# Kernel tuning notes

Measured on AMD Instinct MI355X. Metric: run time of the kernel, lower is better.

## Reference

```python
import jax, jax.numpy as jnp
import numpy as np
import math

NUM_HEADS = 16
D_MODEL = 1024
B, T = 1, 4096


def setup_inputs() -> dict:
    key = jax.random.key(0)
    kx, kq, kk, kv, ko = jax.random.split(key, 5)
    s = 1.0 / math.sqrt(D_MODEL)
    return {
        "x": jax.random.normal(kx, (B, T, D_MODEL), dtype=jnp.float32),
        "Wq": jax.random.normal(kq, (D_MODEL, D_MODEL), dtype=jnp.float32) * s,
        "Wk": jax.random.normal(kk, (D_MODEL, D_MODEL), dtype=jnp.float32) * s,
        "Wv": jax.random.normal(kv, (D_MODEL, D_MODEL), dtype=jnp.float32) * s,
        "Wo": jax.random.normal(ko, (D_MODEL, D_MODEL), dtype=jnp.float32) * s,
    }


def reference(x, Wq, Wk, Wv, Wo):
    # x: (B, T, D); weights stored torch-Linear style: y = x @ W.T
    Bx, Tx, D = x.shape
    H = NUM_HEADS
    dk = D // H
    q = (x @ Wq.T).reshape(Bx, Tx, H, dk)  # (B,T,H,dk)
    k = (x @ Wk.T).reshape(Bx, Tx, H, dk)
    v = (x @ Wv.T).reshape(Bx, Tx, H, dk)
    # scores: (B,H,T,T), scaled dot-product
    scores = jnp.einsum("bthd,bshd->bhts", q, k) / math.sqrt(dk)
    causal_mask = jnp.triu(jnp.ones((Tx, Tx), dtype=bool), k=1)  # True above diag
    scores = jnp.where(causal_mask, jnp.float32(-jnp.inf), scores).astype(jnp.float32)
    attn = jax.nn.softmax(scores, axis=-1)  # fp32 softmax, as in the torch module
    out = jnp.einsum("bhts,bshd->bthd", attn, v).reshape(Bx, Tx, D)
    return out @ Wo.T
```

## Files before the change

### kernel.cpp

```cpp
#include <hip/hip_runtime.h>
#include <hip/hip_bf16.h>
#include <math.h>

typedef __attribute__((ext_vector_type(8)))  __bf16 bf16x8;
typedef __attribute__((ext_vector_type(4)))  __bf16 bf16x4;
typedef __attribute__((ext_vector_type(4)))  float  f32x4;
typedef __attribute__((ext_vector_type(16))) float  f32x16;

static constexpr int T_SEQ = 4096;
static constexpr int DM    = 1024;
static constexpr int NH    = 16;
static constexpr int SPLIT_QB   = 34;
static constexpr int SPLIT_ROWS = T_SEQ - SPLIT_QB * 64;
static constexpr float QSCALE = 0.125f * 1.44269504088896340736f;

__device__ __forceinline__ void gload16(const void* g, void* l) {
    __builtin_amdgcn_global_load_lds(
        (const __attribute__((address_space(1))) unsigned int*)g,
        (__attribute__((address_space(3))) unsigned int*)l,
        16, 0, 0);
}

__device__ __forceinline__ unsigned cvtpk_bf16(float a, float b) {
    unsigned r;
    asm("v_cvt_pk_bf16_f32 %0, %1, %2" : "=v"(r) : "v"(a), "v"(b));
    return r;
}
__device__ __forceinline__ void permswap(unsigned& x, unsigned& y) {
    asm("v_permlane32_swap_b32 %0, %1" : "+v"(x), "+v"(y));
}
__device__ __forceinline__ float xhalf_max(float v) {
    union { float f; unsigned u; } a, b;
    a.f = v; b.f = v;
    asm volatile("" : "+v"(b.u));
    permswap(a.u, b.u);
    return fmaxf(a.f, b.f);
}
__device__ __forceinline__ float xhalf_sum(float v) {
    union { float f; unsigned u; } a, b;
    a.f = v; b.f = v;
    asm volatile("" : "+v"(b.u));
    permswap(a.u, b.u);
    return a.f + b.f;
}

__global__ __launch_bounds__(256)
void cvt_bf16(const float* __restrict__ in, __bf16* __restrict__ out, int n4) {
    int i = blockIdx.x * blockDim.x + threadIdx.x;
    if (i >= n4) return;
    float4 v = ((const float4*)in)[i];
    bf16x4 o;
    o[0] = (__bf16)v.x; o[1] = (__bf16)v.y; o[2] = (__bf16)v.z; o[3] = (__bf16)v.w;
    ((bf16x4*)out)[i] = o;
}

__global__ __launch_bounds__(256)
void cvt4_bf16(const float* __restrict__ a0, const float* __restrict__ a1,
               const float* __restrict__ a2, const float* __restrict__ a3,
               __bf16* __restrict__ o0, __bf16* __restrict__ o1,
               __bf16* __restrict__ o2, __bf16* __restrict__ o3, int n4) {
    int i = blockIdx.x * blockDim.x + threadIdx.x;
    if (i >= n4) return;
    const float* in = blockIdx.y == 0 ? a0 : blockIdx.y == 1 ? a1 : blockIdx.y == 2 ? a2 : a3;
    __bf16* out     = blockIdx.y == 0 ? o0 : blockIdx.y == 1 ? o1 : blockIdx.y == 2 ? o2 : o3;
    float4 v = ((const float4*)in)[i];
    bf16x4 o;
    o[0] = (__bf16)v.x; o[1] = (__bf16)v.y; o[2] = (__bf16)v.z; o[3] = (__bf16)v.w;
    ((bf16x4*)out)[i] = o;
}

template<bool OUT_BF16>
__device__ __forceinline__ void gemm_body(const __bf16* __restrict__ A,
                                          const __bf16* __restrict__ B,
                                          void* __restrict__ Cout,
                                          int N, int K, float scale,
                                          int bx, int by) {
    __shared__ __align__(16) __bf16 Al[128 * 64];
    __shared__ __align__(16) __bf16 Bl[128 * 64];
    const int tid  = threadIdx.x;
    const int lane = tid & 63;
    const int wid  = tid >> 6;
    const int wr   = wid >> 1, wc = wid & 1;
    const int m0   = by * 128, n0 = bx * 128;
    const int r    = lane & 15, g = lane >> 4;

    f32x4 acc[4][4];
    const f32x4 z4 = {0.f, 0.f, 0.f, 0.f};
    #pragma unroll
    for (int i = 0; i < 4; ++i)
        #pragma unroll
        for (int j = 0; j < 4; ++j) acc[i][j] = z4;

    for (int kt = 0; kt < K; kt += 64) {
        __syncthreads();
        #pragma unroll
        for (int p = 0; p < 4; ++p) {
            int u    = p * 256 + tid;
            int row  = u >> 3;
            int col8 = (u & 7) ^ (row & 7);
            gload16(A + (size_t)(m0 + row) * K + kt + col8 * 8,
                    (char*)Al + (p * 256 + wid * 64) * 16);
            gload16(B + (size_t)(n0 + row) * K + kt + col8 * 8,
                    (char*)Bl + (p * 256 + wid * 64) * 16);
        }
        __syncthreads();
        __builtin_amdgcn_s_setprio(1);
        #pragma unroll
        for (int kk = 0; kk < 2; ++kk) {
            bf16x8 af[4], bfr[4];
            #pragma unroll
            for (int mi = 0; mi < 4; ++mi)
                af[mi] = *(const bf16x8*)&Al[(wr * 64 + mi * 16 + r) * 64 + (((kk * 4 + g) ^ (r & 7)) * 8)];
            #pragma unroll
            for (int nj = 0; nj < 4; ++nj)
                bfr[nj] = *(const bf16x8*)&Bl[(wc * 64 + nj * 16 + r) * 64 + (((kk * 4 + g) ^ (r & 7)) * 8)];
            #pragma unroll
            for (int mi = 0; mi < 4; ++mi)
                #pragma unroll
                for (int nj = 0; nj < 4; ++nj)
                    acc[mi][nj] = __builtin_amdgcn_mfma_f32_16x16x32_bf16(af[mi], bfr[nj], acc[mi][nj], 0, 0, 0);
        }
        __builtin_amdgcn_s_setprio(0);
    }
    #pragma unroll
    for (int mi = 0; mi < 4; ++mi)
        #pragma unroll
        for (int nj = 0; nj < 4; ++nj)
            #pragma unroll
            for (int j = 0; j < 4; ++j) {
                int row = m0 + wr * 64 + mi * 16 + g * 4 + j;
                int col = n0 + wc * 64 + nj * 16 + r;
                float v = acc[mi][nj][j] * scale;
                if (OUT_BF16) ((__bf16*)Cout)[(size_t)row * N + col] = (__bf16)v;
                else          ((float*)Cout)[(size_t)row * N + col]  = v;
            }
}

__global__ __launch_bounds__(256)
void gemm_qkv(const __bf16* __restrict__ A,
              const __bf16* __restrict__ W0, const __bf16* __restrict__ W1,
              const __bf16* __restrict__ W2,
              __bf16* __restrict__ O0, __bf16* __restrict__ O1, __bf16* __restrict__ O2) {
    const int z = blockIdx.z;
    const __bf16* B = z == 0 ? W0 : (z == 1 ? W1 : W2);
    __bf16*       C = z == 0 ? O0 : (z == 1 ? O1 : O2);
    float scale = z == 0 ? QSCALE : 1.0f;
    gemm_body<true>(A, B, C, DM, DM, scale, blockIdx.x, blockIdx.y);
}

__global__ __launch_bounds__(256)
void gemm_out(const __bf16* __restrict__ A, const __bf16* __restrict__ B,
              float* __restrict__ C) {
    gemm_body<false>(A, B, C, DM, DM, 1.0f, blockIdx.x, blockIdx.y);
}

__global__ __launch_bounds__(256)
void vtrans(const __bf16* __restrict__ V, __bf16* __restrict__ Vt) {
    __shared__ __bf16 tl[64][72];
    const int tid = threadIdx.x;
    const int t0  = blockIdx.x * 64;
    const int h   = blockIdx.y;
    #pragma unroll
    for (int p = 0; p < 2; ++p) {
        int c = p * 256 + tid, row = c >> 3, col8 = c & 7;
        *(bf16x8*)&tl[row][col8 * 8] =
            *(const bf16x8*)(V + (size_t)(t0 + row) * DM + h * 64 + col8 * 8);
    }
    __syncthreads();
    #pragma unroll
    for (int p = 0; p < 2; ++p) {
        int c = p * 256 + tid, d = c >> 3, tc8 = c & 7;
        bf16x8 o;
        #pragma unroll
        for (int e = 0; e < 8; ++e) o[e] = tl[tc8 * 8 + e][d];
        *(bf16x8*)(Vt + (size_t)(h * 64 + d) * T_SEQ + t0 + tc8 * 8) = o;
    }
}

__global__ __launch_bounds__(128)
void attn_fwd(const __bf16* __restrict__ Q, const __bf16* __restrict__ Kp,
              const __bf16* __restrict__ Vt, __bf16* __restrict__ O,
              __bf16* __restrict__ U, float* __restrict__ Ml)
{
    __shared__ __align__(16) __bf16 Kl[2][64 * 64];
    __shared__ __align__(16) __bf16 Vl[2][64 * 64];
    const int tid  = threadIdx.x;
    const int lane = tid & 63, wid = tid >> 6;
    const int l31  = lane & 31;
    const int hi   = lane >> 5;
    const int h    = blockIdx.x;
    const int y    = blockIdx.y;
    int qb, t0i, t1i, chunk;
    bool split;
    if (y < SPLIT_QB) {
        qb = (SPLIT_QB - 1) - y; t0i = 0; t1i = qb; split = false; chunk = 0;
    } else {
        int s = y - SPLIT_QB;
        qb = 63 - (s >> 1);
        int n = qb + 1, c0 = n - (n >> 1);
        split = true;
        if ((s & 1) == 0) { chunk = 0; t0i = 0;  t1i = c0 - 1; }
        else              { chunk = 1; t0i = c0; t1i = qb;     }
    }
    const int qw = qb * 64 + wid * 32;
    const int qg = qw + l31;

    bf16x8 qf[4];
    #pragma unroll
    for (int kd0 = 0; kd0 < 4; ++kd0)
        qf[kd0] = *(const bf16x8*)(Q + (size_t)qg * DM + h * 64 + kd0 * 16 + hi * 8);

    float m_i = -1e30f, l_i = 0.f;
    f32x16 oacc[2];
    #pragma unroll
    for (int d = 0; d < 2; ++d)
        #pragma unroll
        for (int e = 0; e < 16; ++e) oacc[d][e] = 0.f;

    auto stage_lds = [&](int t, int buf) {
        #pragma unroll
        for (int p = 0; p < 4; ++p) {
            int u    = p * 128 + tid;
            int row  = u >> 3;
            int col8 = (u & 7) ^ (row & 7);
            gload16(Kp + (size_t)(t * 64 + row) * DM + h * 64 + col8 * 8,
                    (char*)&Kl[buf][0] + (p * 128 + wid * 64) * 16);
            gload16(Vt + (size_t)(h * 64 + row) * T_SEQ + t * 64 + col8 * 8,
                    (char*)&Vl[buf][0] + (p * 128 + wid * 64) * 16);
        }
    };
    stage_lds(t0i, 0);
    if (t1i > t0i) stage_lds(t0i + 1, 1);
    __syncthreads();

    auto qk = [&](f32x16* sdst, int buf) {
        #pragma unroll
        for (int ksub = 0; ksub < 2; ++ksub) {
            const int row = ksub * 32 + l31;
            f32x16 a;
            #pragma unroll
            for (int e = 0; e < 16; ++e) a[e] = 0.f;
            #pragma unroll
            for (int kd0 = 0; kd0 < 4; ++kd0) {
                bf16x8 kf = *(const bf16x8*)
                    &Kl[buf][(row << 6) + ((((kd0 << 1) + hi) ^ (row & 7)) << 3)];
                a = __builtin_amdgcn_mfma_f32_32x32x16_bf16(kf, qf[kd0], a, 0, 0, 0);
            }
            sdst[ksub] = a;
        }
    };
    auto mask_sf = [&](f32x16* s, int t) {
        const int kb = (t << 6) + 4 * hi;
        #pragma unroll
        for (int ksub = 0; ksub < 2; ++ksub)
            #pragma unroll
            for (int e = 0; e < 16; ++e) {
                int k = kb + ksub * 32 + ((e & 3) + 8 * (e >> 2));
                if (k > qg) s[ksub][e] = -1e30f;
            }
    };

    f32x16 sf[2], sfn[2];
    qk(sf, 0);
    if (t0i == qb) mask_sf(sf, t0i);

    bf16x8 kreg[4], vreg[4];
    for (int t = t0i; t <= t1i; ++t) {
        const int cur = (t - t0i) & 1;
        const bool have_next  = (t + 1 <= t1i);
        const bool have_next2 = (t + 2 <= t1i);
        if (have_next2) {
            const int t2 = t + 2;
            #pragma unroll
            for (int p = 0; p < 4; ++p) {
                int u   = p * 128 + tid;
                int row = u >> 3;
                int c   = u & 7;
                kreg[p] = *(const bf16x8*)(Kp + (size_t)(t2 * 64 + row) * DM + h * 64 + c * 8);
                vreg[p] = *(const bf16x8*)(Vt + (size_t)(h * 64 + row) * T_SEQ + t2 * 64 + c * 8);
            }
        }
        __builtin_amdgcn_s_setprio(1);
        if (have_next) {
            qk(sfn, cur ^ 1);
            if (t + 1 == qb) mask_sf(sfn, t + 1);
        }
        __builtin_amdgcn_s_setprio(0);
        float pm;
        {
            float t0[8];
            #pragma unroll
            for (int e = 0; e < 8; ++e)
                t0[e] = fmaxf(fmaxf(sf[0][e], sf[0][e + 8]), fmaxf(sf[1][e], sf[1][e + 8]));
            #pragma unroll
            for (int s = 4; s > 0; s >>= 1)
                #pragma unroll
                for (int e = 0; e < s; ++e) t0[e] = fmaxf(t0[e], t0[e + s]);
            pm = xhalf_max(t0[0]);
        }
        if (pm > m_i + 8.f) {
            float al = exp2f(m_i - pm);
            m_i = pm;
            l_i *= al;
            #pragma unroll
            for (int d = 0; d < 2; ++d)
                #pragma unroll
                for (int e = 0; e < 16; ++e) oacc[d][e] *= al;
        }
        float p[32];
        #pragma unroll
        for (int i = 0; i < 32; ++i)
            p[i] = exp2f(sf[i >> 4][i & 15] - m_i);
        {
            float s0[8];
            #pragma unroll
            for (int e = 0; e < 8; ++e)
                s0[e] = (p[e] + p[e + 8]) + (p[e + 16] + p[e + 24]);
            #pragma unroll
            for (int s = 4; s > 0; s >>= 1)
                #pragma unroll
                for (int e = 0; e < s; ++e) s0[e] += s0[e + s];
            l_i += xhalf_sum(s0[0]);
        }
        __builtin_amdgcn_s_setprio(1);
        #pragma unroll
        for (int ks = 0; ks < 4; ++ks) {
            unsigned w0 = cvtpk_bf16(p[8 * ks + 0], p[8 * ks + 1]);
            unsigned w1 = cvtpk_bf16(p[8 * ks + 2], p[8 * ks + 3]);
            unsigned w2 = cvtpk_bf16(p[8 * ks + 4], p[8 * ks + 5]);
            unsigned w3 = cvtpk_bf16(p[8 * ks + 6], p[8 * ks + 7]);
            permswap(w0, w2);
            permswap(w1, w3);
            union { unsigned u[4]; bf16x8 v; } pu;
            pu.u[0] = w0; pu.u[1] = w1; pu.u[2] = w2; pu.u[3] = w3;
            #pragma unroll
            for (int dsub = 0; dsub < 2; ++dsub) {
                const int row = dsub * 32 + l31;
                bf16x8 vt = *(const bf16x8*)
                    &Vl[cur][(row << 6) + ((((ks << 1) + hi) ^ (row & 7)) << 3)];
                oacc[dsub] = __builtin_amdgcn_mfma_f32_32x32x16_bf16(vt, pu.v, oacc[dsub], 0, 0, 0);
            }
        }
        __builtin_amdgcn_s_setprio(0);
        if (have_next2) {
            __syncthreads();
            #pragma unroll
            for (int p = 0; p < 4; ++p) {
                int u   = p * 128 + tid;
                int row = u >> 3;
                int c   = u & 7;
                *(bf16x8*)&Kl[cur][(row << 6) + ((c ^ (row & 7)) << 3)] = kreg[p];
                *(bf16x8*)&Vl[cur][(row << 6) + ((c ^ (row & 7)) << 3)] = vreg[p];
            }
            __syncthreads();
        }
        if (have_next) {
            sf[0] = sfn[0];
            sf[1] = sfn[1];
        }
    }
    __syncthreads();
    __bf16* ow = &Kl[0][0] + wid * 2048;
    const float invl = split ? 1.0f : (1.f / l_i);
    #pragma unroll
    for (int dsub = 0; dsub < 2; ++dsub)
        #pragma unroll
        for (int e = 0; e < 16; ++e) {
            int d = dsub * 32 + ((e & 3) + 8 * (e >> 2)) + 4 * hi;
            float v = oacc[dsub][e] * invl;
            int bo = l31 * 128 + ((2 * d) ^ ((l31 & 7) << 4));
            *(__bf16*)((char*)ow + bo) = (__bf16)v;
        }
    if (!split) {
        #pragma unroll
        for (int i = 0; i < 4; ++i) {
            int u  = hi * 4 + i;
            int bo = l31 * 128 + ((u * 16) ^ ((l31 & 7) << 4));
            bf16x8 v8 = *(const bf16x8*)((char*)ow + bo);
            *(bf16x8*)(O + (size_t)qg * DM + h * 64 + u * 8) = v8;
        }
    } else {
        const int ridx = qg - SPLIT_QB * 64;
        #pragma unroll
        for (int i = 0; i < 4; ++i) {
            int u  = hi * 4 + i;
            int bo = l31 * 128 + ((u * 16) ^ ((l31 & 7) << 4));
            bf16x8 v8 = *(const bf16x8*)((char*)ow + bo);
            *(bf16x8*)(U + ((size_t)(chunk * NH + h) * SPLIT_ROWS + ridx) * 64 + u * 8) = v8;
        }
        if (hi == 0) {
            float* mlp = Ml + ((size_t)(chunk * NH + h) * SPLIT_ROWS + ridx) * 2;
            mlp[0] = m_i;
            mlp[1] = l_i;
        }
    }
}

__global__ __launch_bounds__(256)
void attn_combine(const __bf16* __restrict__ U, const float* __restrict__ Ml,
                  __bf16* __restrict__ O) {
    int gid = blockIdx.x * 256 + threadIdx.x;
    int rh  = gid >> 3;
    int e8  = gid & 7;
    int ridx = rh >> 4, h = rh & 15;
    const float* ml0 = Ml + ((size_t)(0 * NH + h) * SPLIT_ROWS + ridx) * 2;
    const float* ml1 = Ml + ((size_t)(1 * NH + h) * SPLIT_ROWS + ridx) * 2;
    float m0 = ml0[0], l0 = ml0[1], m1 = ml1[0], l1 = ml1[1];
    float M  = fmaxf(m0, m1);
    float s0 = exp2f(m0 - M), s1 = exp2f(m1 - M);
    float inv = 1.f / (l0 * s0 + l1 * s1);
    bf16x8 u0 = *(const bf16x8*)(U + ((size_t)(0 * NH + h) * SPLIT_ROWS + ridx) * 64 + e8 * 8);
    bf16x8 u1 = *(const bf16x8*)(U + ((size_t)(1 * NH + h) * SPLIT_ROWS + ridx) * 64 + e8 * 8);
    bf16x8 o;
    #pragma unroll
    for (int j = 0; j < 8; ++j)
        o[j] = (__bf16)(((float)u0[j] * s0 + (float)u1[j] * s1) * inv);
    *(bf16x8*)(O + (size_t)(SPLIT_QB * 64 + ridx) * DM + h * 64 + e8 * 8) = o;
}

extern "C" void kernel_launch(void* const* d_in, const int* in_sizes, int n_in,
                              void* d_out, int out_size, void* d_ws, size_t ws_size,
                              hipStream_t stream) {
    const float* x  = (const float*)d_in[0];
    const float* Wq = (const float*)d_in[1];
    const float* Wk = (const float*)d_in[2];
    const float* Wv = (const float*)d_in[3];
    const float* Wo = (const float*)d_in[4];
    float* out = (float*)d_out;

    char* ws = (char*)d_ws;
    const size_t MB = (size_t)1 << 20;
    __bf16* xb    = (__bf16*)(ws + 0 * MB);
    __bf16* VtG   = (__bf16*)(ws + 0 * MB);
    __bf16* wqb   = (__bf16*)(ws + 8 * MB);
    float*  MlB   = (float*)(ws + 8 * MB);
    __bf16* wkb   = (__bf16*)(ws + 10 * MB);
    __bf16* wvb   = (__bf16*)(ws + 12 * MB);
    __bf16* wob   = (__bf16*)(ws + 14 * MB);
    __bf16* Qb    = (__bf16*)(ws + 16 * MB);
    __bf16* Kb    = (__bf16*)(ws + 24 * MB);
    __bf16* Vb    = (__bf16*)(ws + 32 * MB);
    __bf16* UB    = (__bf16*)(ws + 32 * MB);
    __bf16* attnb = (__bf16*)(ws + 40 * MB);

    const int nX = T_SEQ * DM / 4;
    const int nW = DM * DM / 4;
    cvt_bf16<<<(nX + 255) / 256, 256, 0, stream>>>(x, xb, nX);
    cvt4_bf16<<<dim3((nW + 255) / 256, 4), 256, 0, stream>>>(Wq, Wk, Wv, Wo,
                                                             wqb, wkb, wvb, wob, nW);

    gemm_qkv<<<dim3(DM / 128, T_SEQ / 128, 3), 256, 0, stream>>>(xb, wqb, wkb, wvb, Qb, Kb, Vb);

    vtrans<<<dim3(T_SEQ / 64, NH), 256, 0, stream>>>(Vb, VtG);

    attn_fwd<<<dim3(NH, SPLIT_QB + 2 * (64 - SPLIT_QB)), 128, 0, stream>>>(
        Qb, Kb, VtG, attnb, UB, MlB);

    attn_combine<<<(SPLIT_ROWS * NH * 8) / 256, 256, 0, stream>>>(UB, MlB, attnb);

    gemm_out<<<dim3(DM / 128, T_SEQ / 128), 256, 0, stream>>>(attnb, wob, out);
}
```

Measured before the change: 165.2 us.

## Fuse V transpose into QKV GEMM and restructure attention loop pipelining

The V projection GEMM now writes its output transposed, which removes the separate vtrans kernel and its extra round trip through global memory. The attention kernel drops register-staged prefetch of the next-next tile and the software-pipelined QK in favour of direct LDS staging (global_load_lds) of the next tile with one barrier per iteration. The row-sum of P is now computed by an extra MFMA against a ones vector instead of a VALU reduction. The block order is changed so that split (long) query blocks are scheduled first, and the max reduction uses three-input max. Together these cut launch count and VALU work, but lose some overlap between QK compute and loads.

```diff
diff --git a/kernel.cpp b/kernel.cpp
--- a/kernel.cpp
+++ b/kernel.cpp
@@ -12,6 +12,7 @@
 static constexpr int NH    = 16;
 static constexpr int SPLIT_QB   = 34;
 static constexpr int SPLIT_ROWS = T_SEQ - SPLIT_QB * 64;
+static constexpr int NSPLIT_Y   = 2 * (64 - SPLIT_QB);
 static constexpr float QSCALE = 0.125f * 1.44269504088896340736f;
 
 __device__ __forceinline__ void gload16(const void* g, void* l) {
@@ -42,6 +43,9 @@
     asm volatile("" : "+v"(b.u));
     permswap(a.u, b.u);
     return a.f + b.f;
+}
+__device__ __forceinline__ float max3f(float a, float b, float c) {
+    return fmaxf(fmaxf(a, b), c);
 }
 
 __global__ __launch_bounds__(256)
@@ -69,7 +73,7 @@
     ((bf16x4*)out)[i] = o;
 }
 
-template<bool OUT_BF16>
+template<int MODE>
 __device__ __forceinline__ void gemm_body(const __bf16* __restrict__ A,
                                           const __bf16* __restrict__ B,
                                           void* __restrict__ Cout,
@@ -125,56 +129,42 @@
     #pragma unroll
     for (int mi = 0; mi < 4; ++mi)
         #pragma unroll
-        for (int nj = 0; nj < 4; ++nj)
-            #pragma unroll
-            for (int j = 0; j < 4; ++j) {
-                int row = m0 + wr * 64 + mi * 16 + g * 4 + j;
-                int col = n0 + wc * 64 + nj * 16 + r;
-                float v = acc[mi][nj][j] * scale;
-                if (OUT_BF16) ((__bf16*)Cout)[(size_t)row * N + col] = (__bf16)v;
-                else          ((float*)Cout)[(size_t)row * N + col]  = v;
+        for (int nj = 0; nj < 4; ++nj) {
+            if (MODE == 2) {
+                int rowb = m0 + wr * 64 + mi * 16 + g * 4;
+                int col  = n0 + wc * 64 + nj * 16 + r;
+                bf16x4 o;
+                #pragma unroll
+                for (int j = 0; j < 4; ++j) o[j] = (__bf16)(acc[mi][nj][j] * scale);
+                *(bf16x4*)((__bf16*)Cout + (size_t)col * T_SEQ + rowb) = o;
+            } else {
+                #pragma unroll
+                for (int j = 0; j < 4; ++j) {
+                    int row = m0 + wr * 64 + mi * 16 + g * 4 + j;
+                    int col = n0 + wc * 64 + nj * 16 + r;
+                    float v = acc[mi][nj][j] * scale;
+                    if (MODE == 1) ((__bf16*)Cout)[(size_t)row * N + col] = (__bf16)v;
+                    else           ((float*)Cout)[(size_t)row * N + col]  = v;
+                }
             }
+        }
 }
 
 __global__ __launch_bounds__(256)
 void gemm_qkv(const __bf16* __restrict__ A,
               const __bf16* __restrict__ W0, const __bf16* __restrict__ W1,
               const __bf16* __restrict__ W2,
-              __bf16* __restrict__ O0, __bf16* __restrict__ O1, __bf16* __restrict__ O2) {
+              __bf16* __restrict__ O0, __bf16* __restrict__ O1, __bf16* __restrict__ Vt) {
     const int z = blockIdx.z;
-    const __bf16* B = z == 0 ? W0 : (z == 1 ? W1 : W2);
-    __bf16*       C = z == 0 ? O0 : (z == 1 ? O1 : O2);
-    float scale = z == 0 ? QSCALE : 1.0f;
-    gemm_body<true>(A, B, C, DM, DM, scale, blockIdx.x, blockIdx.y);
+    if (z == 0)      gemm_body<1>(A, W0, O0, DM, DM, QSCALE, blockIdx.x, blockIdx.y);
+    else if (z == 1) gemm_body<1>(A, W1, O1, DM, DM, 1.0f,   blockIdx.x, blockIdx.y);
+    else             gemm_body<2>(A, W2, Vt, DM, DM, 1.0f,   blockIdx.x, blockIdx.y);
 }
 
 __global__ __launch_bounds__(256)
 void gemm_out(const __bf16* __restrict__ A, const __bf16* __restrict__ B,
               float* __restrict__ C) {
-    gemm_body<false>(A, B, C, DM, DM, 1.0f, blockIdx.x, blockIdx.y);
-}
-
-__global__ __launch_bounds__(256)
-void vtrans(const __bf16* __restrict__ V, __bf16* __restrict__ Vt) {
-    __shared__ __bf16 tl[64][72];
-    const int tid = threadIdx.x;
-    const int t0  = blockIdx.x * 64;
-    const int h   = blockIdx.y;
-    #pragma unroll
-    for (int p = 0; p < 2; ++p) {
-        int c = p * 256 + tid, row = c >> 3, col8 = c & 7;
-        *(bf16x8*)&tl[row][col8 * 8] =
-            *(const bf16x8*)(V + (size_t)(t0 + row) * DM + h * 64 + col8 * 8);
-    }
-    __syncthreads();
-    #pragma unroll
-    for (int p = 0; p < 2; ++p) {
-        int c = p * 256 + tid, d = c >> 3, tc8 = c & 7;
-        bf16x8 o;
-        #pragma unroll
-        for (int e = 0; e < 8; ++e) o[e] = tl[tc8 * 8 + e][d];
-        *(bf16x8*)(Vt + (size_t)(h * 64 + d) * T_SEQ + t0 + tc8 * 8) = o;
-    }
+    gemm_body<0>(A, B, C, DM, DM, 1.0f, blockIdx.x, blockIdx.y);
 }
 
 __global__ __launch_bounds__(128)
@@ -192,15 +182,15 @@
     const int y    = blockIdx.y;
     int qb, t0i, t1i, chunk;
     bool split;
-    if (y < SPLIT_QB) {
-        qb = (SPLIT_QB - 1) - y; t0i = 0; t1i = qb; split = false; chunk = 0;
-    } else {
-        int s = y - SPLIT_QB;
-        qb = 63 - (s >> 1);
+    if (y < NSPLIT_Y) {
+        qb = 63 - (y >> 1);
         int n = qb + 1, c0 = n - (n >> 1);
         split = true;
-        if ((s & 1) == 0) { chunk = 0; t0i = 0;  t1i = c0 - 1; }
+        if ((y & 1) == 0) { chunk = 0; t0i = 0;  t1i = c0 - 1; }
         else              { chunk = 1; t0i = c0; t1i = qb;     }
+    } else {
+        qb = (SPLIT_QB - 1) - (y - NSPLIT_Y);
+        t0i = 0; t1i = qb; split = false; chunk = 0;
     }
     const int qw = qb * 64 + wid * 32;
     const int qg = qw + l31;
@@ -210,12 +200,21 @@
     for (int kd0 = 0; kd0 < 4; ++kd0)
         qf[kd0] = *(const bf16x8*)(Q + (size_t)qg * DM + h * 64 + kd0 * 16 + hi * 8);
 
-    float m_i = -1e30f, l_i = 0.f;
-    f32x16 oacc[2];
+    bf16x8 onesA;
+    {
+        __bf16 ov = (__bf16)((l31 == 0) ? 1.0f : 0.0f);
+        #pragma unroll
+        for (int e = 0; e < 8; ++e) onesA[e] = ov;
+    }
+
+    float m_i = -1e30f;
+    f32x16 oacc[2], lacc;
     #pragma unroll
     for (int d = 0; d < 2; ++d)
         #pragma unroll
         for (int e = 0; e < 16; ++e) oacc[d][e] = 0.f;
+    #pragma unroll
+    for (int e = 0; e < 16; ++e) lacc[e] = 0.f;
 
     auto stage_lds = [&](int t, int buf) {
         #pragma unroll
@@ -230,10 +229,13 @@
         }
     };
     stage_lds(t0i, 0);
-    if (t1i > t0i) stage_lds(t0i + 1, 1);
-    __syncthreads();
-
-    auto qk = [&](f32x16* sdst, int buf) {
+
+    for (int t = t0i; t <= t1i; ++t) {
+        const int cur = (t - t0i) & 1;
+        __syncthreads();
+        if (t < t1i) stage_lds(t + 1, cur ^ 1);
+        f32x16 sf[2];
+        __builtin_amdgcn_s_setprio(1);
         #pragma unroll
         for (int ksub = 0; ksub < 2; ++ksub) {
             const int row = ksub * 32 + l31;
@@ -243,65 +245,37 @@
             #pragma unroll
             for (int kd0 = 0; kd0 < 4; ++kd0) {
                 bf16x8 kf = *(const bf16x8*)
-                    &Kl[buf][(row << 6) + ((((kd0 << 1) + hi) ^ (row & 7)) << 3)];
+                    &Kl[cur][(row << 6) + ((((kd0 << 1) + hi) ^ (row & 7)) << 3)];
                 a = __builtin_amdgcn_mfma_f32_32x32x16_bf16(kf, qf[kd0], a, 0, 0, 0);
             }
-            sdst[ksub] = a;
-        }
-    };
-    auto mask_sf = [&](f32x16* s, int t) {
-        const int kb = (t << 6) + 4 * hi;
-        #pragma unroll
-        for (int ksub = 0; ksub < 2; ++ksub)
-            #pragma unroll
-            for (int e = 0; e < 16; ++e) {
-                int k = kb + ksub * 32 + ((e & 3) + 8 * (e >> 2));
-                if (k > qg) s[ksub][e] = -1e30f;
-            }
-    };
-
-    f32x16 sf[2], sfn[2];
-    qk(sf, 0);
-    if (t0i == qb) mask_sf(sf, t0i);
-
-    bf16x8 kreg[4], vreg[4];
-    for (int t = t0i; t <= t1i; ++t) {
-        const int cur = (t - t0i) & 1;
-        const bool have_next  = (t + 1 <= t1i);
-        const bool have_next2 = (t + 2 <= t1i);
-        if (have_next2) {
-            const int t2 = t + 2;
-            #pragma unroll
-            for (int p = 0; p < 4; ++p) {
-                int u   = p * 128 + tid;
-                int row = u >> 3;
-                int c   = u & 7;
-                kreg[p] = *(const bf16x8*)(Kp + (size_t)(t2 * 64 + row) * DM + h * 64 + c * 8);
-                vreg[p] = *(const bf16x8*)(Vt + (size_t)(h * 64 + row) * T_SEQ + t2 * 64 + c * 8);
-            }
-        }
-        __builtin_amdgcn_s_setprio(1);
-        if (have_next) {
-            qk(sfn, cur ^ 1);
-            if (t + 1 == qb) mask_sf(sfn, t + 1);
+            sf[ksub] = a;
         }
         __builtin_amdgcn_s_setprio(0);
+        if (t == qb) {
+            const int kb = (t << 6) + 4 * hi;
+            #pragma unroll
+            for (int ksub = 0; ksub < 2; ++ksub)
+                #pragma unroll
+                for (int e = 0; e < 16; ++e) {
+                    int k = kb + ksub * 32 + ((e & 3) + 8 * (e >> 2));
+                    if (k > qg) sf[ksub][e] = -1e30f;
+                }
+        }
         float pm;
         {
-            float t0[8];
+            float t8[8];
             #pragma unroll
             for (int e = 0; e < 8; ++e)
-                t0[e] = fmaxf(fmaxf(sf[0][e], sf[0][e + 8]), fmaxf(sf[1][e], sf[1][e + 8]));
-            #pragma unroll
-            for (int s = 4; s > 0; s >>= 1)
-                #pragma unroll
-                for (int e = 0; e < s; ++e) t0[e] = fmaxf(t0[e], t0[e + s]);
-            pm = xhalf_max(t0[0]);
+                t8[e] = fmaxf(max3f(sf[0][e], sf[0][e + 8], sf[1][e]), sf[1][e + 8]);
+            float u0 = max3f(t8[0], t8[1], t8[2]);
+            float u1 = max3f(t8[3], t8[4], t8[5]);
+            float u2 = max3f(t8[6], t8[7], u0);
+            pm = xhalf_max(fmaxf(u1, u2));
         }
         if (pm > m_i + 8.f) {
             float al = exp2f(m_i - pm);
             m_i = pm;
-            l_i *= al;
+            lacc[0] *= al;
             #pragma unroll
             for (int d = 0; d < 2; ++d)
                 #pragma unroll
@@ -311,17 +285,6 @@
         #pragma unroll
         for (int i = 0; i < 32; ++i)
             p[i] = exp2f(sf[i >> 4][i & 15] - m_i);
-        {
-            float s0[8];
-            #pragma unroll
-            for (int e = 0; e < 8; ++e)
-                s0[e] = (p[e] + p[e + 8]) + (p[e + 16] + p[e + 24]);
-            #pragma unroll
-            for (int s = 4; s > 0; s >>= 1)
-                #pragma unroll
-                for (int e = 0; e < s; ++e) s0[e] += s0[e + s];
-            l_i += xhalf_sum(s0[0]);
-        }
         __builtin_amdgcn_s_setprio(1);
         #pragma unroll
         for (int ks = 0; ks < 4; ++ks) {
@@ -340,28 +303,14 @@
                     &Vl[cur][(row << 6) + ((((ks << 1) + hi) ^ (row & 7)) << 3)];
                 oacc[dsub] = __builtin_amdgcn_mfma_f32_32x32x16_bf16(vt, pu.v, oacc[dsub], 0, 0, 0);
             }
+            lacc = __builtin_amdgcn_mfma_f32_32x32x16_bf16(onesA, pu.v, lacc, 0, 0, 0);
         }
         __builtin_amdgcn_s_setprio(0);
-        if (have_next2) {
-            __syncthreads();
-            #pragma unroll
-            for (int p = 0; p < 4; ++p) {
-                int u   = p * 128 + tid;
-                int row = u >> 3;
-                int c   = u & 7;
-                *(bf16x8*)&Kl[cur][(row << 6) + ((c ^ (row & 7)) << 3)] = kreg[p];
-                *(bf16x8*)&Vl[cur][(row << 6) + ((c ^ (row & 7)) << 3)] = vreg[p];
-            }
-            __syncthreads();
-        }
-        if (have_next) {
-            sf[0] = sfn[0];
-            sf[1] = sfn[1];
-        }
     }
+    const float l_v = xhalf_sum(lacc[0]);
     __syncthreads();
     __bf16* ow = &Kl[0][0] + wid * 2048;
-    const float invl = split ? 1.0f : (1.f / l_i);
+    const float invl = split ? 1.0f : (1.f / l_v);
     #pragma unroll
     for (int dsub = 0; dsub < 2; ++dsub)
         #pragma unroll
@@ -391,7 +340,7 @@
         if (hi == 0) {
             float* mlp = Ml + ((size_t)(chunk * NH + h) * SPLIT_ROWS + ridx) * 2;
             mlp[0] = m_i;
-            mlp[1] = l_i;
+            mlp[1] = l_v;
         }
     }
 }
@@ -431,7 +380,7 @@
     char* ws = (char*)d_ws;
     const size_t MB = (size_t)1 << 20;
     __bf16* xb    = (__bf16*)(ws + 0 * MB);
-    __bf16* VtG   = (__bf16*)(ws + 0 * MB);
+    __bf16* UB    = (__bf16*)(ws + 0 * MB);
     __bf16* wqb   = (__bf16*)(ws + 8 * MB);
     float*  MlB   = (float*)(ws + 8 * MB);
     __bf16* wkb   = (__bf16*)(ws + 10 * MB);
@@ -439,8 +388,7 @@
     __bf16* wob   = (__bf16*)(ws + 14 * MB);
     __bf16* Qb    = (__bf16*)(ws + 16 * MB);
     __bf16* Kb    = (__bf16*)(ws + 24 * MB);
-    __bf16* Vb    = (__bf16*)(ws + 32 * MB);
-    __bf16* UB    = (__bf16*)(ws + 32 * MB);
+    __bf16* VtB   = (__bf16*)(ws + 32 * MB);
     __bf16* attnb = (__bf16*)(ws + 40 * MB);
 
     const int nX = T_SEQ * DM / 4;
@@ -449,12 +397,11 @@
     cvt4_bf16<<<dim3((nW + 255) / 256, 4), 256, 0, stream>>>(Wq, Wk, Wv, Wo,
                                                              wqb, wkb, wvb, wob, nW);
 
-    gemm_qkv<<<dim3(DM / 128, T_SEQ / 128, 3), 256, 0, stream>>>(xb, wqb, wkb, wvb, Qb, Kb, Vb);
-
-    vtrans<<<dim3(T_SEQ / 64, NH), 256, 0, stream>>>(Vb, VtG);
-
-    attn_fwd<<<dim3(NH, SPLIT_QB + 2 * (64 - SPLIT_QB)), 128, 0, stream>>>(
-        Qb, Kb, VtG, attnb, UB, MlB);
+    gemm_qkv<<<dim3(DM / 128, T_SEQ / 128, 3), 256, 0, stream>>>(xb, wqb, wkb, wvb,
+                                                                 Qb, Kb, VtB);
+
+    attn_fwd<<<dim3(NH, NSPLIT_Y + SPLIT_QB), 128, 0, stream>>>(
+        Qb, Kb, VtB, attnb, UB, MlB);
 
     attn_combine<<<(SPLIT_ROWS * NH * 8) / 256, 256, 0, stream>>>(UB, MlB, attnb);
 
```

After: 179.8 us. +8.8%, slower.
